# Kernel optimization log

Measured on AMD Instinct MI355X. Metric: run time of the kernel, lower is better.

## Reference

```python
import jax, jax.numpy as jnp
import numpy as np

B, S, H, R, NH = 4, 2048, 1024, 512, 8
HD = R // NH
EPS = 1e-5


def _ln(x, g, b):
    m = jnp.mean(x, axis=-1, keepdims=True)
    v = jnp.mean(jnp.square(x - m), axis=-1, keepdims=True)
    return (x - m) * jax.lax.rsqrt(v + EPS) * g + b


def setup_inputs() -> dict:
    key = jax.random.key(0)
    ks = iter(jax.random.split(key, 40))
    s = 0.02
    d = {}
    d['hidden_states'] = jax.random.normal(next(ks), (B, S, H), dtype=jnp.float32)
    # complexity assessor: H -> H//4 -> 32 -> 1
    d['ca_w1'] = jax.random.normal(next(ks), (H, H // 4)) * s
    d['ca_b1'] = jnp.zeros((H // 4,))
    d['ca_w2'] = jax.random.normal(next(ks), (H // 4, 32)) * s
    d['ca_b2'] = jnp.zeros((32,))
    d['ca_w3'] = jax.random.normal(next(ks), (32, 1)) * s
    d['ca_b3'] = jnp.zeros((1,))
    # reasoning projection H -> R, and pre-norm
    d['rp_w'] = jax.random.normal(next(ks), (H, R)) * s
    d['rp_b'] = jnp.zeros((R,))
    d['rn_g'] = jnp.ones((R,)); d['rn_b'] = jnp.zeros((R,))
    # transformer encoder layer (norm_first)
    d['ln1_g'] = jnp.ones((R,)); d['ln1_b'] = jnp.zeros((R,))
    d['wqkv'] = jax.random.normal(next(ks), (R, 3 * R)) * s
    d['bqkv'] = jnp.zeros((3 * R,))
    d['wo'] = jax.random.normal(next(ks), (R, R)) * s
    d['bo'] = jnp.zeros((R,))
    d['ln2_g'] = jnp.ones((R,)); d['ln2_b'] = jnp.zeros((R,))
    d['ff1_w'] = jax.random.normal(next(ks), (R, 4 * R)) * s
    d['ff1_b'] = jnp.zeros((4 * R,))
    d['ff2_w'] = jax.random.normal(next(ks), (4 * R, R)) * s
    d['ff2_b'] = jnp.zeros((R,))
    # output projection R -> H and norm
    d['op_w'] = jax.random.normal(next(ks), (R, H)) * s
    d['op_b'] = jnp.zeros((H,))
    d['on_g'] = jnp.ones((H,)); d['on_b'] = jnp.zeros((H,))
    # integration gate: 2H -> H -> H
    d['gw1'] = jax.random.normal(next(ks), (2 * H, H)) * s
    d['gb1'] = jnp.zeros((H,))
    d['gw2'] = jax.random.normal(next(ks), (H, H)) * s
    d['gb2'] = jnp.zeros((H,))
    return d


def reference(hidden_states, ca_w1, ca_b1, ca_w2, ca_b2, ca_w3, ca_b3,
              rp_w, rp_b, rn_g, rn_b, ln1_g, ln1_b, wqkv, bqkv, wo, bo,
              ln2_g, ln2_b, ff1_w, ff1_b, ff2_w, ff2_b, op_w, op_b,
              on_g, on_b, gw1, gb1, gw2, gb2):
    # complexity assessment (metrics only; input_ids=None forces reasoning on all)
    pooled = jnp.mean(hidden_states, axis=1)  # [B,H]
    h = jax.nn.relu(pooled @ ca_w1 + ca_b1)
    h = jax.nn.relu(h @ ca_w2 + ca_b2)
    complexity_scores = jax.nn.sigmoid(h @ ca_w3 + ca_b3)[:, 0]  # [B]

    # apply_reasoning on full batch (should_reason is all-True)
    r = _ln(hidden_states @ rp_w + rp_b, rn_g, rn_b)  # [B,S,R]

    # TransformerEncoderLayer, norm_first, relu, dropout=0
    y = _ln(r, ln1_g, ln1_b)
    qkv = y @ wqkv + bqkv
    q, k, v = jnp.split(qkv, 3, axis=-1)
    q = q.reshape(B, S, NH, HD)
    k = k.reshape(B, S, NH, HD)
    v = v.reshape(B, S, NH, HD)
    scores = jnp.einsum('bqhd,bkhd->bhqk', q, k) / np.sqrt(HD).astype(np.float32)
    attn = jax.nn.softmax(scores, axis=-1)
    o = jnp.einsum('bhqk,bkhd->bqhd', attn, v).reshape(B, S, R)
    r = r + (o @ wo + bo)
    y = _ln(r, ln2_g, ln2_b)
    r = r + (jax.nn.relu(y @ ff1_w + ff1_b) @ ff2_w + ff2_b)

    reasoned = _ln(r @ op_w + op_b, on_g, on_b)  # [B,S,H]

    # sigmoid integration gate on concat([states, reasoned])
    gate_in = jnp.concatenate([hidden_states, reasoned], axis=-1)
    g = jax.nn.relu(gate_in @ gw1 + gb1)
    g = jax.nn.sigmoid(g @ gw2 + gb2)
    output = hidden_states + g * reasoned
    return output, complexity_scores
```

## Files before the change

### kernel.cpp

```cpp
#include <hip/hip_runtime.h>
#include <hip/hip_bf16.h>
#include <math.h>


typedef __bf16 bf16;
typedef __attribute__((ext_vector_type(8))) __bf16 bf16x8;
typedef __attribute__((ext_vector_type(4))) float f32x4;
typedef __attribute__((ext_vector_type(16))) float f32x16;

__device__ __forceinline__ void glds16(const bf16* g, bf16* l) {
  __builtin_amdgcn_global_load_lds(
      (const __attribute__((address_space(1))) void*)g,
      (__attribute__((address_space(3))) void*)l, 16, 0, 0);
}

struct TD { const float* src; char* dst; int rows, cols, tx, start, outbf; };
struct TDs { TD d[9]; };
__global__ void k_trans_all(TDs td) {
  int bid = blockIdx.x;
  int si = 0;
  for (int i = 1; i < 9; i++)
    if (bid >= td.d[i].start) si = i;
  TD dd = td.d[si];
  int tid = bid - dd.start;
  int bx = tid % dd.tx, by = tid / dd.tx;
  __shared__ float tile[32][33];
  int c0 = bx * 32, r0 = by * 32;
  int tx = threadIdx.x, ty = threadIdx.y;
  for (int i = 0; i < 32; i += 8)
    tile[ty + i][tx] = dd.src[(long)(r0 + ty + i) * dd.cols + (c0 + tx)];
  __syncthreads();
  if (dd.outbf) {
    bf16* o = (bf16*)dd.dst;
    for (int i = 0; i < 32; i += 8)
      o[(long)(c0 + ty + i) * dd.rows + (r0 + tx)] = (bf16)tile[tx][ty + i];
  } else {
    float* o = (float*)dd.dst;
    for (int i = 0; i < 32; i += 8)
      o[(long)(c0 + ty + i) * dd.rows + (r0 + tx)] = tile[tx][ty + i];
  }
}

__global__ void k_cvt(const float* __restrict__ in, bf16* __restrict__ out) {
  long i = ((long)blockIdx.x * 256 + threadIdx.x) * 4;
  float4 v = *(const float4*)(in + i);
  bf16* o = out + i;
  o[0] = (bf16)v.x; o[1] = (bf16)v.y; o[2] = (bf16)v.z; o[3] = (bf16)v.w;
}

__global__ void k_vtrans(const bf16* __restrict__ qkv, bf16* __restrict__ VT) {
  __shared__ bf16 tile[32][33];
  int bh = blockIdx.z, b = bh >> 3, h = bh & 7;
  const bf16* in = qkv + (long)b * 2048 * 1536 + 1024 + h * 64;
  bf16* out = VT + (long)bh * 64 * 2048;
  int c0 = blockIdx.x * 32, r0 = blockIdx.y * 32;
  int tx = threadIdx.x, ty = threadIdx.y;
  for (int i = 0; i < 32; i += 8)
    tile[ty + i][tx] = in[(long)(r0 + ty + i) * 1536 + (c0 + tx)];
  __syncthreads();
  for (int i = 0; i < 32; i += 8)
    out[(long)(c0 + ty + i) * 2048 + (r0 + tx)] = tile[tx][ty + i];
}

__global__ void k_pool_part(const float* __restrict__ X, float* __restrict__ part) {
  int b = blockIdx.y, c = blockIdx.z;
  int col = blockIdx.x * 256 + threadIdx.x;
  const float* p = X + (long)b * 2048 * 1024 + (long)c * 128 * 1024 + col;
  float s = 0.f;
  for (int i = 0; i < 128; i++) s += p[(long)i * 1024];
  part[((long)c * 4 + b) * 1024 + col] = s;
}

__global__ void k_pool_fin(const float* __restrict__ part, float* __restrict__ pooled) {
  int idx = blockIdx.x * 256 + threadIdx.x;
  int b = idx >> 10, col = idx & 1023;
  float s = 0.f;
  for (int c = 0; c < 16; c++) s += part[((long)c * 4 + b) * 1024 + col];
  pooled[idx] = s * (1.0f / 2048.0f);
}

__global__ void k_ca1(const float* __restrict__ pooled, const float* __restrict__ w1T,
                      const float* __restrict__ b1, float* __restrict__ h1) {
  int t = blockIdx.x, b = threadIdx.x >> 6, lane = threadIdx.x & 63;
  const float* wr = w1T + (long)t * 1024 + lane * 16;
  const float* pr = pooled + b * 1024 + lane * 16;
  float acc = 0.f;
  for (int j = 0; j < 4; j++) {
    float4 w = *(const float4*)(wr + j * 4);
    float4 p = *(const float4*)(pr + j * 4);
    acc += w.x * p.x + w.y * p.y + w.z * p.z + w.w * p.w;
  }
  for (int off = 32; off; off >>= 1) acc += __shfl_xor(acc, off);
  if (lane == 0) h1[b * 256 + t] = fmaxf(acc + b1[t], 0.f);
}

__global__ void k_ca2(const float* __restrict__ h1,
                      const float* __restrict__ w2, const float* __restrict__ b2,
                      const float* __restrict__ w3, const float* __restrict__ b3,
                      float* __restrict__ scores) {
  __shared__ float w2s[256 * 32];
  __shared__ float h1s[4 * 256];
  __shared__ float h2s[4][32];
  int t = threadIdx.x;
  for (int j = 0; j < 32; j++) w2s[j * 256 + t] = w2[j * 256 + t];
  for (int j = 0; j < 4; j++) h1s[j * 256 + t] = h1[j * 256 + t];
  __syncthreads();
  if (t < 128) {
    int b = t >> 5, o = t & 31;
    float acc = b2[o];
    for (int k = 0; k < 256; k++) acc += h1s[b * 256 + k] * w2s[k * 32 + o];
    h2s[b][o] = fmaxf(acc, 0.f);
  }
  __syncthreads();
  if (t < 4) {
    float acc = b3[0];
    for (int k = 0; k < 32; k++) acc += h2s[t][k] * w3[k];
    scores[t] = 1.f / (1.f + expf(-acc));
  }
}

template <int NCOL>
__global__ void k_ln(const bf16* __restrict__ in, const float* __restrict__ g,
                     const float* __restrict__ be, bf16* __restrict__ out) {
  int wave = threadIdx.x >> 6, lane = threadIdx.x & 63;
  long row = (long)blockIdx.x * 4 + wave;
  const bf16* x = in + row * NCOL;
  constexpr int PER = NCOL / 64;
  constexpr int CH = PER / 8;
  float v[PER];
  float s = 0.f;
  for (int c = 0; c < CH; c++) {
    bf16x8 t = *(const bf16x8*)(x + c * 512 + lane * 8);
    for (int j = 0; j < 8; j++) { v[c * 8 + j] = (float)t[j]; s += v[c * 8 + j]; }
  }
  for (int off = 32; off; off >>= 1) s += __shfl_xor(s, off);
  float mean = s * (1.0f / NCOL);
  float q = 0.f;
  for (int i = 0; i < PER; i++) { float d = v[i] - mean; q += d * d; }
  for (int off = 32; off; off >>= 1) q += __shfl_xor(q, off);
  float rstd = rsqrtf(q * (1.0f / NCOL) + 1e-5f);
  for (int c = 0; c < CH; c++) {
    bf16x8 o;
    for (int j = 0; j < 8; j++) {
      int col = c * 512 + lane * 8 + j;
      o[j] = (bf16)((v[c * 8 + j] - mean) * rstd * g[col] + be[col]);
    }
    *(bf16x8*)(out + row * NCOL + c * 512 + lane * 8) = o;
  }
}

__global__ void k_ln2(const bf16* __restrict__ in,
                      const float* __restrict__ g1, const float* __restrict__ b1,
                      const float* __restrict__ g2, const float* __restrict__ b2,
                      bf16* __restrict__ outR, bf16* __restrict__ outY) {
  int wave = threadIdx.x >> 6, lane = threadIdx.x & 63;
  long row = (long)blockIdx.x * 4 + wave;
  const bf16* x = in + row * 512;
  float v[8];
  float s = 0.f;
  bf16x8 t = *(const bf16x8*)(x + lane * 8);
  for (int j = 0; j < 8; j++) { v[j] = (float)t[j]; s += v[j]; }
  for (int off = 32; off; off >>= 1) s += __shfl_xor(s, off);
  float mean = s * (1.0f / 512);
  float q = 0.f;
  for (int j = 0; j < 8; j++) { float d = v[j] - mean; q += d * d; }
  for (int off = 32; off; off >>= 1) q += __shfl_xor(q, off);
  float rstd = rsqrtf(q * (1.0f / 512) + 1e-5f);
  float r[8];
  float s2 = 0.f;
  bf16x8 orr;
  for (int j = 0; j < 8; j++) {
    int col = lane * 8 + j;
    r[j] = (v[j] - mean) * rstd * g1[col] + b1[col];
    orr[j] = (bf16)r[j];
    s2 += r[j];
  }
  *(bf16x8*)(outR + row * 512 + lane * 8) = orr;
  for (int off = 32; off; off >>= 1) s2 += __shfl_xor(s2, off);
  float mean2 = s2 * (1.0f / 512);
  float q2 = 0.f;
  for (int j = 0; j < 8; j++) { float d = r[j] - mean2; q2 += d * d; }
  for (int off = 32; off; off >>= 1) q2 += __shfl_xor(q2, off);
  float rstd2 = rsqrtf(q2 * (1.0f / 512) + 1e-5f);
  bf16x8 oy;
  for (int j = 0; j < 8; j++) {
    int col = lane * 8 + j;
    oy[j] = (bf16)((r[j] - mean2) * rstd2 * g2[col] + b2[col]);
  }
  *(bf16x8*)(outY + row * 512 + lane * 8) = oy;
}

template <int EPI, int MT>
__launch_bounds__(256, 2)
__global__ void k_gemm(const bf16* __restrict__ A1, int ldA1,
                       const bf16* __restrict__ B1, int ldB1, int K1,
                       const bf16* __restrict__ A2, int ldA2,
                       const bf16* __restrict__ B2, int ldB2, int K2,
                       const float* __restrict__ bias, void* __restrict__ out,
                       int ldOut, const bf16* __restrict__ resid, int ldRes,
                       const float* __restrict__ auxX, const bf16* __restrict__ auxR) {
  __shared__ __align__(16) bf16 As[MT * 32];
  __shared__ __align__(16) bf16 Bs[128 * 32];
  constexpr int NF = (MT == 128) ? 4 : 2;
  constexpr int NW = (MT == 128) ? 64 : 32;
  int t = threadIdx.x;
  int wave = t >> 6, lane = t & 63, quad = lane >> 4, l16 = lane & 15;
  int wy = (MT == 128) ? (wave >> 1) : 0;
  int wx = (MT == 128) ? (wave & 1) : wave;
  int m0 = blockIdx.y * MT, n0 = blockIdx.x * 128;
  int sr = t >> 2;
  int sc = (t & 3) * 8;
  bf16* la0 = As + wave * 512;
  bf16* la1 = As + 2048 + wave * 512;
  bf16* lb0 = Bs + wave * 512;
  bf16* lb1 = Bs + 2048 + wave * 512;

  f32x4 acc[4][NF] = {};

  auto run = [&](const bf16* A, int ldA, const bf16* Bt, int ldB, int K) {
    const bf16* ag0 = A + (long)(m0 + sr) * ldA + sc;
    const bf16* ag1 = ag0 + (long)64 * ldA;
    const bf16* bg0 = Bt + (long)(n0 + sr) * ldB + sc;
    const bf16* bg1 = bg0 + (long)64 * ldB;
    for (int kt = 0; kt < K; kt += 32) {
      glds16(ag0 + kt, la0);
      if constexpr (MT == 128) glds16(ag1 + kt, la1);
      glds16(bg0 + kt, lb0);
      glds16(bg1 + kt, lb1);
      __syncthreads();
      bf16x8 af[4], bfr[NF];
      for (int im = 0; im < 4; im++)
        af[im] = *(const bf16x8*)(As + (64 * wy + 16 * im + l16) * 32 + quad * 8);
      for (int in = 0; in < NF; in++)
        bfr[in] = *(const bf16x8*)(Bs + (NW * wx + 16 * in + l16) * 32 + quad * 8);
      for (int im = 0; im < 4; im++)
        for (int in = 0; in < NF; in++)
          acc[im][in] = __builtin_amdgcn_mfma_f32_16x16x32_bf16(af[im], bfr[in],
                                                                acc[im][in], 0, 0, 0);
      __syncthreads();
    }
  };
  run(A1, ldA1, B1, ldB1, K1);
  if (A2) run(A2, ldA2, B2, ldB2, K2);

  int rb = m0 + 64 * wy + quad * 4;
  int cb = n0 + NW * wx + l16;
  for (int im = 0; im < 4; im++)
    for (int in = 0; in < NF; in++)
      for (int i = 0; i < 4; i++) {
        int row = rb + 16 * im + i;
        int col = cb + 16 * in;
        long o = (long)row * ldOut + col;
        float v = acc[im][in][i] + bias[col];
        if constexpr (EPI == 0) ((bf16*)out)[o] = (bf16)v;
        else if constexpr (EPI == 1) ((bf16*)out)[o] = (bf16)fmaxf(v, 0.f);
        else if constexpr (EPI == 2)
          ((bf16*)out)[o] = (bf16)(v + (float)resid[(long)row * ldRes + col]);
        else {
          float gg = 1.f / (1.f + expf(-v));
          ((float*)out)[o] = auxX[o] + gg * (float)auxR[o];
        }
      }
}

__launch_bounds__(256, 2)
__global__ void k_attn(const bf16* __restrict__ qkv, const bf16* __restrict__ VT,
                       bf16* __restrict__ o_out) {
  __shared__ __align__(16) bf16 Ks[64 * 72];
  __shared__ __align__(16) bf16 Vs[64 * 72];
  __shared__ __align__(16) bf16 PQs[128 * 72];
  int t = threadIdx.x, wave = t >> 6, lane = t & 63;
  int l32 = lane & 31, half = lane >> 5;
  int q0 = blockIdx.x * 128;
  int h = blockIdx.y, b = blockIdx.z;
  const bf16* qb = qkv + (long)b * 2048 * 1536 + h * 64;
  const bf16* vb = VT + (long)(b * 8 + h) * 64 * 2048;

  for (int i = 0; i < 4; i++) {
    int idx = i * 256 + t, q = idx >> 3, cg = idx & 7;
    *(uint4*)(PQs + q * 72 + cg * 8) =
        *(const uint4*)(qb + (long)(q0 + q) * 1536 + cg * 8);
  }
  __syncthreads();
  bf16x8 qf[4];
  for (int c = 0; c < 4; c++)
    qf[c] = *(const bf16x8*)(PQs + (wave * 32 + l32) * 72 + c * 16 + half * 8);

  float rs[16];
  for (int i = 0; i < 16; i++) rs[i] = 0.f;
  f32x16 oacc[2] = {};
  const float scale = 0.125f;

  for (int kt = 0; kt < 32; kt++) {
    int k0 = kt * 64;
    __syncthreads();
    for (int i = 0; i < 2; i++) {
      int idx = i * 256 + t, r = idx >> 3, cg = idx & 7;
      *(uint4*)(Ks + r * 72 + cg * 8) =
          *(const uint4*)(qb + 512 + (long)(k0 + r) * 1536 + cg * 8);
      *(uint4*)(Vs + r * 72 + cg * 8) =
          *(const uint4*)(vb + (long)r * 2048 + k0 + cg * 8);
    }
    __syncthreads();

    for (int kb = 0; kb < 2; kb++) {
      f32x16 s = {};
      for (int c = 0; c < 4; c++) {
        bf16x8 kf = *(const bf16x8*)(Ks + (kb * 32 + l32) * 72 + c * 16 + half * 8);
        s = __builtin_amdgcn_mfma_f32_32x32x16_bf16(qf[c], kf, s, 0, 0, 0);
      }
      for (int r = 0; r < 16; r++) {
        float p = __expf(s[r] * scale);
        rs[r] += p;
        int row = (r & 3) + 8 * (r >> 2) + 4 * half;
        PQs[(wave * 32 + row) * 72 + kb * 32 + l32] = (bf16)p;
      }
    }
    for (int c = 0; c < 4; c++) {
      bf16x8 pf = *(const bf16x8*)(PQs + (wave * 32 + l32) * 72 + c * 16 + half * 8);
      for (int db = 0; db < 2; db++) {
        bf16x8 vf = *(const bf16x8*)(Vs + (db * 32 + l32) * 72 + c * 16 + half * 8);
        oacc[db] = __builtin_amdgcn_mfma_f32_32x32x16_bf16(pf, vf, oacc[db], 0, 0, 0);
      }
    }
  }
  for (int r = 0; r < 16; r++)
    for (int off = 1; off < 32; off <<= 1) rs[r] += __shfl_xor(rs[r], off);
  for (int r = 0; r < 16; r++) {
    float inv = 1.f / rs[r];
    int row = q0 + wave * 32 + (r & 3) + 8 * (r >> 2) + 4 * half;
    long gr = ((long)b * 2048 + row) * 512 + h * 64;
    o_out[gr + l32] = (bf16)(oacc[0][r] * inv);
    o_out[gr + 32 + l32] = (bf16)(oacc[1][r] * inv);
  }
}

extern "C" void kernel_launch(void* const* d_in, const int* in_sizes, int n_in,
                              void* d_out, int out_size, void* d_ws, size_t ws_size,
                              hipStream_t stream) {
  const float* X    = (const float*)d_in[0];
  const float* caw1 = (const float*)d_in[1];
  const float* cab1 = (const float*)d_in[2];
  const float* caw2 = (const float*)d_in[3];
  const float* cab2 = (const float*)d_in[4];
  const float* caw3 = (const float*)d_in[5];
  const float* cab3 = (const float*)d_in[6];
  const float* rp_w = (const float*)d_in[7];
  const float* rp_b = (const float*)d_in[8];
  const float* rn_g = (const float*)d_in[9];
  const float* rn_b = (const float*)d_in[10];
  const float* ln1g = (const float*)d_in[11];
  const float* ln1b = (const float*)d_in[12];
  const float* wqkv = (const float*)d_in[13];
  const float* bqkv = (const float*)d_in[14];
  const float* wo   = (const float*)d_in[15];
  const float* bo   = (const float*)d_in[16];
  const float* ln2g = (const float*)d_in[17];
  const float* ln2b = (const float*)d_in[18];
  const float* ff1w = (const float*)d_in[19];
  const float* ff1b = (const float*)d_in[20];
  const float* ff2w = (const float*)d_in[21];
  const float* ff2b = (const float*)d_in[22];
  const float* opw  = (const float*)d_in[23];
  const float* opb  = (const float*)d_in[24];
  const float* ong  = (const float*)d_in[25];
  const float* onb  = (const float*)d_in[26];
  const float* gw1  = (const float*)d_in[27];
  const float* gb1  = (const float*)d_in[28];
  const float* gw2  = (const float*)d_in[29];
  const float* gb2  = (const float*)d_in[30];

  char* ws = (char*)d_ws;
  const size_t MB = 1u << 20;
  const size_t KB = 1u << 10;
  bf16* rpwT  = (bf16*)ws;
  bf16* wqkvT = rpwT + 524288;
  bf16* woT   = wqkvT + 786432;
  bf16* ff1T  = woT + 262144;
  bf16* ff2T  = ff1T + 1048576;
  bf16* opT   = ff2T + 1048576;
  bf16* gw1T  = opT + 524288;
  bf16* gw2T  = gw1T + 2097152;
  float* part   = (float*)(ws + 14 * MB);
  float* pooled = (float*)(ws + 14 * MB + 256 * KB);
  float* h1buf  = (float*)(ws + 14 * MB + 272 * KB);
  bf16* Xb   = (bf16*)(ws + 15 * MB);
  bf16* bufA = (bf16*)(ws + 31 * MB);
  bf16* bufB = (bf16*)(ws + 39 * MB);
  bf16* bufC = (bf16*)(ws + 47 * MB);
  bf16* qkv  = (bf16*)(ws + 55 * MB);
  float* w1T = (float*)(ws + 55 * MB);
  bf16* VT   = (bf16*)(ws + 79 * MB);
  bf16* f1   = (bf16*)(ws + 55 * MB);
  bf16* tmp3 = (bf16*)(ws + 55 * MB);
  bf16* rsn  = (bf16*)(ws + 71 * MB);
  bf16* g1   = (bf16*)(ws + 31 * MB);

  TDs td;
  td.d[0] = {rp_w, (char*)rpwT, 1024, 512, 16, 0, 1};
  td.d[1] = {wqkv, (char*)wqkvT, 512, 1536, 48, 512, 1};
  td.d[2] = {wo, (char*)woT, 512, 512, 16, 1280, 1};
  td.d[3] = {ff1w, (char*)ff1T, 512, 2048, 64, 1536, 1};
  td.d[4] = {ff2w, (char*)ff2T, 2048, 512, 16, 2560, 1};
  td.d[5] = {opw, (char*)opT, 512, 1024, 32, 3584, 1};
  td.d[6] = {gw1, (char*)gw1T, 2048, 1024, 32, 4096, 1};
  td.d[7] = {gw2, (char*)gw2T, 1024, 1024, 32, 6144, 1};
  td.d[8] = {caw1, (char*)w1T, 1024, 256, 8, 7168, 0};
  dim3 b32x8(32, 8);
  k_trans_all<<<7424, b32x8, 0, stream>>>(td);
  k_cvt<<<8192, 256, 0, stream>>>(X, Xb);

  k_pool_part<<<dim3(4, 4, 16), 256, 0, stream>>>(X, part);
  k_pool_fin<<<16, 256, 0, stream>>>(part, pooled);
  k_ca1<<<256, 256, 0, stream>>>(pooled, w1T, cab1, h1buf);
  k_ca2<<<1, 256, 0, stream>>>(h1buf, caw2, cab2, caw3, cab3,
                               (float*)d_out + 8388608);

  k_gemm<0, 64><<<dim3(4, 128), 256, 0, stream>>>(
      Xb, 1024, rpwT, 1024, 1024, nullptr, 0, nullptr, 0, 0,
      rp_b, bufA, 512, nullptr, 0, nullptr, nullptr);
  k_ln2<<<2048, 256, 0, stream>>>(bufA, rn_g, rn_b, ln1g, ln1b, bufB, bufC);
  k_gemm<0, 128><<<dim3(12, 64), 256, 0, stream>>>(
      bufC, 512, wqkvT, 512, 512, nullptr, 0, nullptr, 0, 0,
      bqkv, qkv, 1536, nullptr, 0, nullptr, nullptr);
  k_vtrans<<<dim3(2, 64, 32), b32x8, 0, stream>>>(qkv, VT);
  k_attn<<<dim3(16, 8, 4), 256, 0, stream>>>(qkv, VT, bufC);
  k_gemm<2, 64><<<dim3(4, 128), 256, 0, stream>>>(
      bufC, 512, woT, 512, 512, nullptr, 0, nullptr, 0, 0,
      bo, bufA, 512, bufB, 512, nullptr, nullptr);
  k_ln<512><<<2048, 256, 0, stream>>>(bufA, ln2g, ln2b, bufB);
  k_gemm<1, 128><<<dim3(16, 64), 256, 0, stream>>>(
      bufB, 512, ff1T, 512, 512, nullptr, 0, nullptr, 0, 0,
      ff1b, f1, 2048, nullptr, 0, nullptr, nullptr);
  k_gemm<2, 64><<<dim3(4, 128), 256, 0, stream>>>(
      f1, 2048, ff2T, 2048, 2048, nullptr, 0, nullptr, 0, 0,
      ff2b, bufC, 512, bufA, 512, nullptr, nullptr);
  k_gemm<0, 128><<<dim3(8, 64), 256, 0, stream>>>(
      bufC, 512, opT, 512, 512, nullptr, 0, nullptr, 0, 0,
      opb, tmp3, 1024, nullptr, 0, nullptr, nullptr);
  k_ln<1024><<<2048, 256, 0, stream>>>(tmp3, ong, onb, rsn);
  k_gemm<1, 128><<<dim3(8, 64), 256, 0, stream>>>(
      Xb, 1024, gw1T, 2048, 1024, rsn, 1024, gw1T + 1024, 2048, 1024,
      gb1, g1, 1024, nullptr, 0, nullptr, nullptr);
  k_gemm<5, 128><<<dim3(8, 64), 256, 0, stream>>>(
      g1, 1024, gw2T, 1024, 1024, nullptr, 0, nullptr, 0, 0,
      gb2, (float*)d_out, 1024, nullptr, 0, X, rsn);
}
```

Measured before the change: 511.2 us.

## Split attention over two key halves and merge with a combine kernel

Result: faster. 487.7 us (-4.6%).

```diff
diff --git a/kernel.cpp b/kernel.cpp
--- a/kernel.cpp
+++ b/kernel.cpp
@@ -263,18 +263,20 @@
       }
 }
 
-__launch_bounds__(256, 2)
+__launch_bounds__(256, 4)
 __global__ void k_attn(const bf16* __restrict__ qkv, const bf16* __restrict__ VT,
-                       bf16* __restrict__ o_out) {
+                       bf16* __restrict__ Op0, bf16* __restrict__ Op1,
+                       float* __restrict__ lp) {
   __shared__ __align__(16) bf16 Ks[64 * 72];
   __shared__ __align__(16) bf16 Vs[64 * 72];
   __shared__ __align__(16) bf16 PQs[128 * 72];
   int t = threadIdx.x, wave = t >> 6, lane = t & 63;
   int l32 = lane & 31, half = lane >> 5;
   int q0 = blockIdx.x * 128;
-  int h = blockIdx.y, b = blockIdx.z;
+  int h = blockIdx.y >> 1, split = blockIdx.y & 1, b = blockIdx.z;
   const bf16* qb = qkv + (long)b * 2048 * 1536 + h * 64;
   const bf16* vb = VT + (long)(b * 8 + h) * 64 * 2048;
+  bf16* Op = split ? Op1 : Op0;
 
   for (int i = 0; i < 4; i++) {
     int idx = i * 256 + t, q = idx >> 3, cg = idx & 7;
@@ -291,7 +293,7 @@
   f32x16 oacc[2] = {};
   const float scale = 0.125f;
 
-  for (int kt = 0; kt < 32; kt++) {
+  for (int kt = split * 16; kt < split * 16 + 16; kt++) {
     int k0 = kt * 64;
     __syncthreads();
     for (int i = 0; i < 2; i++) {
@@ -329,10 +331,28 @@
   for (int r = 0; r < 16; r++) {
     float inv = 1.f / rs[r];
     int row = q0 + wave * 32 + (r & 3) + 8 * (r >> 2) + 4 * half;
-    long gr = ((long)b * 2048 + row) * 512 + h * 64;
-    o_out[gr + l32] = (bf16)(oacc[0][r] * inv);
-    o_out[gr + 32 + l32] = (bf16)(oacc[1][r] * inv);
-  }
+    long grow = (long)b * 2048 + row;
+    long gr = grow * 512 + h * 64;
+    Op[gr + l32] = (bf16)(oacc[0][r] * inv);
+    Op[gr + 32 + l32] = (bf16)(oacc[1][r] * inv);
+    if (l32 == 0) lp[(split << 16) + grow * 8 + h] = rs[r];
+  }
+}
+
+__global__ void k_attn_fin(const bf16* __restrict__ O0, const bf16* __restrict__ O1,
+                           const float* __restrict__ lp, bf16* __restrict__ out) {
+  long idx = (long)blockIdx.x * 256 + threadIdx.x;
+  long row = idx >> 6;
+  int c8 = (int)(idx & 63);
+  int h = c8 >> 3;
+  float l0 = lp[row * 8 + h], l1 = lp[65536 + row * 8 + h];
+  float inv = 1.f / (l0 + l1);
+  float w0 = l0 * inv, w1 = l1 * inv;
+  bf16x8 a = *(const bf16x8*)(O0 + idx * 8);
+  bf16x8 bb = *(const bf16x8*)(O1 + idx * 8);
+  bf16x8 o;
+  for (int j = 0; j < 8; j++) o[j] = (bf16)((float)a[j] * w0 + (float)bb[j] * w1);
+  *(bf16x8*)(out + idx * 8) = o;
 }
 
 extern "C" void kernel_launch(void* const* d_in, const int* in_sizes, int n_in,
@@ -382,8 +402,9 @@
   bf16* gw1T  = opT + 524288;
   bf16* gw2T  = gw1T + 2097152;
   float* part   = (float*)(ws + 14 * MB);
-  float* pooled = (float*)(ws + 14 * MB + 256 * KB);
-  float* h1buf  = (float*)(ws + 14 * MB + 272 * KB);
+  float* lpart  = (float*)(ws + 14 * MB);
+  float* pooled = (float*)(ws + 14 * MB + 512 * KB);
+  float* h1buf  = (float*)(ws + 14 * MB + 528 * KB);
   bf16* Xb   = (bf16*)(ws + 15 * MB);
   bf16* bufA = (bf16*)(ws + 31 * MB);
   bf16* bufB = (bf16*)(ws + 39 * MB);
@@ -424,7 +445,8 @@
       bufC, 512, wqkvT, 512, 512, nullptr, 0, nullptr, 0, 0,
       bqkv, qkv, 1536, nullptr, 0, nullptr, nullptr);
   k_vtrans<<<dim3(2, 64, 32), b32x8, 0, stream>>>(qkv, VT);
-  k_attn<<<dim3(16, 8, 4), 256, 0, stream>>>(qkv, VT, bufC);
+  k_attn<<<dim3(16, 16, 4), 256, 0, stream>>>(qkv, VT, bufA, bufC, lpart);
+  k_attn_fin<<<2048, 256, 0, stream>>>(bufA, bufC, lpart, bufC);
   k_gemm<2, 64><<<dim3(4, 128), 256, 0, stream>>>(
       bufC, 512, woT, 512, 512, nullptr, 0, nullptr, 0, 0,
       bo, bufA, 512, bufB, 512, nullptr, nullptr);
```
